# Performance work log

Measured on AMD Instinct MI355X. Metric: run time of the kernel, lower is better.

## Reference

```python
import jax, jax.numpy as jnp
import numpy as np

EPS_LOG = 1e-8
EPS_CHECK = 1e-4


def to_float8(x, exp_bits=4, mant_bits=3):
    # fp8 emulation: sign/abs/log2/floor/clamp/round chain
    max_exp = 2 ** (exp_bits - 1) - 1
    min_exp = -max_exp
    scale = 2.0 ** mant_bits
    sign = jnp.sign(x)
    x_abs = jnp.abs(x)
    exp = jnp.clip(jnp.floor(jnp.log2(x_abs + EPS_LOG)), min_exp, max_exp)
    pow2 = jnp.exp2(exp)
    mant = x_abs / pow2 - 1.0
    mant_q = jnp.round(mant * scale) / scale
    return sign * (1.0 + mant_q) * pow2


def checksum_verify(left, right, epsilon=EPS_CHECK):
    # ABFT: augment left with a column-sum row, right with a row-sum column
    left_cs = jnp.concatenate([left, jnp.sum(left, axis=0, keepdims=True)], axis=0)
    right_cs = jnp.concatenate([right, jnp.sum(right, axis=1, keepdims=True)], axis=1)
    prod_cs = left_cs @ right_cs  # [(m+1), (n+1)]
    output = prod_cs[:-1, :-1]
    row_sum_check = prod_cs[:-1, -1]
    col_sum_check = prod_cs[-1, :-1]
    col_diff = jnp.abs(jnp.sum(output, axis=0) - col_sum_check)
    row_diff = jnp.abs(jnp.sum(output, axis=1) - row_sum_check)
    mask = (row_diff > epsilon)[:, None] & (col_diff > epsilon)[None, :]
    return output, mask


def setup_inputs() -> dict:
    key = jax.random.key(0)
    kx, ku, kA, kB, kC = jax.random.split(key, 5)
    batch, n, m, p = 4096, 2048, 1024, 1024
    return {
        "x": jax.random.normal(kx, (batch, n), dtype=jnp.float32),
        "u": jax.random.normal(ku, (batch, m), dtype=jnp.float32),
        "A": jax.random.normal(kA, (n, n), dtype=jnp.float32),
        "B": jax.random.normal(kB, (n, m), dtype=jnp.float32),
        "C": jax.random.normal(kC, (p, n), dtype=jnp.float32),
    }


def reference(x, u, A, B, C):
    int_bits, frac_bits = 4, 3
    Aq = to_float8(A, int_bits, frac_bits)
    Bq = to_float8(B, int_bits, frac_bits)
    left_term, left_mask = checksum_verify(x, Aq.T)
    right_term, right_mask = checksum_verify(u, Bq.T)
    x_next = to_float8(left_term + right_term, int_bits, frac_bits)
    _ = left_mask | right_mask  # mask computed but discarded in forward (as in torch)
    Cq = to_float8(C, int_bits, frac_bits)
    y = to_float8(x_next @ Cq.T, int_bits, frac_bits)
    return (x_next, y)
```

## Files before the change

### kernel.cpp

```cpp
#include <hip/hip_runtime.h>
#include <hip/hip_bf16.h>
#include <stdint.h>

typedef __bf16 bf16_t;
typedef __attribute__((ext_vector_type(8))) __bf16 bf16x8;
typedef __attribute__((ext_vector_type(4))) __bf16 bf16x4;
typedef __attribute__((ext_vector_type(4))) float f32x4;

__device__ __forceinline__ float q8(float v) {
    float a = __builtin_fabsf(v);
    float z = a + 1e-8f;
    int ei = ((__float_as_int(z) >> 23) & 0xff) - 127;
    ei = ei > 7 ? 7 : (ei < -7 ? -7 : ei);
    float p  = __int_as_float((ei + 127) << 23);
    float ip = __int_as_float((127 - ei) << 23);
    float m  = __builtin_fmaf(a, ip, -1.0f);
    float mq = __builtin_rintf(m * 8.0f) * 0.125f;
    float r  = (1.0f + mq) * p;
    return v < 0.0f ? -r : r;
}

__device__ __forceinline__ void gload_lds16(const bf16_t* g, bf16_t* l) {
    __builtin_amdgcn_global_load_lds(
        (__attribute__((address_space(1))) void*)(g),
        (__attribute__((address_space(3))) void*)(l), 16, 0, 0);
}

__global__ void pack_all(const float* __restrict__ x, const float* __restrict__ u,
                         const float* __restrict__ A, const float* __restrict__ B,
                         const float* __restrict__ C,
                         bf16_t* __restrict__ XU, bf16_t* __restrict__ AB,
                         bf16_t* __restrict__ CQ) {
    unsigned bid = blockIdx.x;
    if (bid < 12288u) {
        unsigned row = bid / 3u, piece = bid - row * 3u;
        int col = (piece * 256 + threadIdx.x) * 4;
        float4 v;
        if (col < 2048) v = *(const float4*)&x[(size_t)row * 2048 + col];
        else            v = *(const float4*)&u[(size_t)row * 1024 + (col - 2048)];
        bf16x4 o = { (bf16_t)v.x, (bf16_t)v.y, (bf16_t)v.z, (bf16_t)v.w };
        *(bf16x4*)&XU[(size_t)row * 3072 + col] = o;
    } else if (bid < 18432u) {
        unsigned b = bid - 12288u;
        unsigned row = b / 3u, piece = b - row * 3u;
        int col = (piece * 256 + threadIdx.x) * 4;
        float4 v;
        if (col < 2048) v = *(const float4*)&A[(size_t)row * 2048 + col];
        else            v = *(const float4*)&B[(size_t)row * 1024 + (col - 2048)];
        bf16x4 o = { (bf16_t)q8(v.x), (bf16_t)q8(v.y), (bf16_t)q8(v.z), (bf16_t)q8(v.w) };
        *(bf16x4*)&AB[(size_t)row * 3072 + col] = o;
    } else {
        unsigned b = bid - 18432u;
        unsigned row = b >> 1, piece = b & 1u;
        int col = (piece * 256 + threadIdx.x) * 4;
        float4 v = *(const float4*)&C[(size_t)row * 2048 + col];
        bf16x4 o = { (bf16_t)q8(v.x), (bf16_t)q8(v.y), (bf16_t)q8(v.z), (bf16_t)q8(v.w) };
        *(bf16x4*)&CQ[(size_t)row * 2048 + col] = o;
    }
}

template<int BN, bool DUAL>
__global__ __launch_bounds__(512, 4)
void gemm_q8_kernel(const bf16_t* __restrict__ A, const bf16_t* __restrict__ B,
                    float* __restrict__ outf, bf16_t* __restrict__ outb,
                    int M, int N, int K) {
    constexpr int BM = 128;
    constexpr int BK = 128;
    constexpr int NI = BN / 32;
    constexpr int A_ITS = BM * (BK / 8) / 512;
    constexpr int B_ITS = BN * (BK / 8) / 512;

    __shared__ alignas(16) bf16_t sA[BM * BK];
    __shared__ alignas(16) bf16_t sB[BN * BK];

    const int tid  = threadIdx.x;
    const int lane = tid & 63;
    const int wave = tid >> 6;
    const int wm   = wave & 3;
    const int wn   = wave >> 2;
    const int ln16 = lane & 15;
    const int quad = lane >> 4;

    const int b   = blockIdx.x;
    const int xcd = b & 7;
    const int g   = b >> 3;
    const int bx  = (xcd & 1) * 8 + (g & 7);
    const int by  = (xcd >> 1) * 8 + (g >> 3);
    const int brow = by * BM;
    const int bcol = bx * BN;

    const bf16_t* gA[A_ITS];
#pragma unroll
    for (int it = 0; it < A_ITS; ++it) {
        int L = it * 512 + tid;
        int r = L >> 4, c = L & 15;
        gA[it] = A + (size_t)(brow + r) * K + (c ^ (r & 15)) * 8;
    }
    const bf16_t* gB[B_ITS];
#pragma unroll
    for (int it = 0; it < B_ITS; ++it) {
        int L = it * 512 + tid;
        int r = L >> 4, c = L & 15;
        gB[it] = B + (size_t)(bcol + r) * K + (c ^ (r & 15)) * 8;
    }

    int a_off[2][4], b_off[NI][4];
#pragma unroll
    for (int im = 0; im < 2; ++im) {
        int r = wm * 32 + im * 16 + ln16;
#pragma unroll
        for (int s = 0; s < 4; ++s) {
            int cg = s * 4 + quad;
            a_off[im][s] = (r * 16 + (cg ^ (r & 15))) * 8;
        }
    }
#pragma unroll
    for (int in = 0; in < NI; ++in) {
        int r = wn * (BN / 2) + in * 16 + ln16;
#pragma unroll
        for (int s = 0; s < 4; ++s) {
            int cg = s * 4 + quad;
            b_off[in][s] = (r * 16 + (cg ^ (r & 15))) * 8;
        }
    }

    f32x4 acc[2][NI];
#pragma unroll
    for (int im = 0; im < 2; ++im)
#pragma unroll
        for (int in = 0; in < NI; ++in)
            acc[im][in] = (f32x4){0.f, 0.f, 0.f, 0.f};

    for (int kt = 0; kt < K; kt += BK) {
#pragma unroll
        for (int it = 0; it < A_ITS; ++it) {
            gload_lds16(gA[it], sA + (it * 512 + wave * 64) * 8);
            gA[it] += BK;
        }
#pragma unroll
        for (int it = 0; it < B_ITS; ++it) {
            gload_lds16(gB[it], sB + (it * 512 + wave * 64) * 8);
            gB[it] += BK;
        }
        __syncthreads();
#pragma unroll
        for (int s = 0; s < 4; ++s) {
            bf16x8 af[2], bfv[NI];
#pragma unroll
            for (int im = 0; im < 2; ++im) af[im]  = *(const bf16x8*)(sA + a_off[im][s]);
#pragma unroll
            for (int in = 0; in < NI; ++in) bfv[in] = *(const bf16x8*)(sB + b_off[in][s]);
#pragma unroll
            for (int im = 0; im < 2; ++im)
#pragma unroll
                for (int in = 0; in < NI; ++in)
                    acc[im][in] = __builtin_amdgcn_mfma_f32_16x16x32_bf16(
                        af[im], bfv[in], acc[im][in], 0, 0, 0);
        }
        __syncthreads();
    }

    const int rbase = quad * 4;
#pragma unroll
    for (int im = 0; im < 2; ++im) {
#pragma unroll
        for (int in = 0; in < NI; ++in) {
            int gm = brow + wm * 32 + im * 16 + rbase;
            int gn = bcol + wn * (BN / 2) + in * 16 + ln16;
#pragma unroll
            for (int r = 0; r < 4; ++r) {
                float v = q8(acc[im][in][r]);
                outf[(size_t)(gm + r) * N + gn] = v;
                if (DUAL) outb[(size_t)(gm + r) * N + gn] = (bf16_t)v;
            }
        }
    }
}

extern "C" void kernel_launch(void* const* d_in, const int* in_sizes, int n_in,
                              void* d_out, int out_size, void* d_ws, size_t ws_size,
                              hipStream_t stream) {
    const float* x = (const float*)d_in[0];
    const float* u = (const float*)d_in[1];
    const float* A = (const float*)d_in[2];
    const float* B = (const float*)d_in[3];
    const float* C = (const float*)d_in[4];

    float* outf = (float*)d_out;
    float* xnf  = outf;
    float* yf   = outf + (size_t)4096 * 2048;

    uint8_t* ws = (uint8_t*)d_ws;
    bf16_t* XU = (bf16_t*)ws;
    bf16_t* AB = (bf16_t*)(ws + (size_t)25165824);
    bf16_t* CQ = (bf16_t*)(ws + (size_t)25165824 + 12582912);
    bf16_t* XN = (bf16_t*)(ws + (size_t)25165824 + 12582912 + 4194304);

    pack_all<<<dim3(20480), 256, 0, stream>>>(x, u, A, B, C, XU, AB, CQ);

    gemm_q8_kernel<128, true><<<dim3(512), 512, 0, stream>>>(
        XU, AB, xnf, XN, 4096, 2048, 3072);
    gemm_q8_kernel<64, false><<<dim3(512), 512, 0, stream>>>(
        XN, CQ, yf, nullptr, 4096, 1024, 2048);
}
```

Measured before the change: 200.6 us.

## Double-buffer GEMM LDS tiles with BK=64 and widen pack loads to 8 elements

The GEMM kernel now keeps two LDS stages with BK=64 and prefetches the next tile while computing the current one, using vmcnt waits and raw barriers in place of a load-then-sync loop. It also raises s_setprio during the MFMA work. The second GEMM switches to 128x128 tiles, which halves its grid to 256 blocks, and the pack kernel handles 8 elements per thread. The aim is to hide global-to-LDS latency and cut per-block overhead, at the cost of more LDS per block, a lower-occupancy second GEMM, and hand-counted waits that must stay correct.

After: 212.0 us. 5.7% more time.

```diff
diff --git a/kernel.cpp b/kernel.cpp
--- a/kernel.cpp
+++ b/kernel.cpp
@@ -4,7 +4,6 @@
 
 typedef __bf16 bf16_t;
 typedef __attribute__((ext_vector_type(8))) __bf16 bf16x8;
-typedef __attribute__((ext_vector_type(4))) __bf16 bf16x4;
 typedef __attribute__((ext_vector_type(4))) float f32x4;
 
 __device__ __forceinline__ float q8(float v) {
@@ -26,52 +25,66 @@
         (__attribute__((address_space(3))) void*)(l), 16, 0, 0);
 }
 
+__device__ __forceinline__ bf16x8 cvt8(float4 a, float4 b) {
+    bf16x8 o = { (bf16_t)a.x, (bf16_t)a.y, (bf16_t)a.z, (bf16_t)a.w,
+                 (bf16_t)b.x, (bf16_t)b.y, (bf16_t)b.z, (bf16_t)b.w };
+    return o;
+}
+__device__ __forceinline__ bf16x8 q8x8(float4 a, float4 b) {
+    bf16x8 o = { (bf16_t)q8(a.x), (bf16_t)q8(a.y), (bf16_t)q8(a.z), (bf16_t)q8(a.w),
+                 (bf16_t)q8(b.x), (bf16_t)q8(b.y), (bf16_t)q8(b.z), (bf16_t)q8(b.w) };
+    return o;
+}
+
 __global__ void pack_all(const float* __restrict__ x, const float* __restrict__ u,
                          const float* __restrict__ A, const float* __restrict__ B,
                          const float* __restrict__ C,
                          bf16_t* __restrict__ XU, bf16_t* __restrict__ AB,
                          bf16_t* __restrict__ CQ) {
-    unsigned bid = blockIdx.x;
-    if (bid < 12288u) {
-        unsigned row = bid / 3u, piece = bid - row * 3u;
-        int col = (piece * 256 + threadIdx.x) * 4;
-        float4 v;
-        if (col < 2048) v = *(const float4*)&x[(size_t)row * 2048 + col];
-        else            v = *(const float4*)&u[(size_t)row * 1024 + (col - 2048)];
-        bf16x4 o = { (bf16_t)v.x, (bf16_t)v.y, (bf16_t)v.z, (bf16_t)v.w };
-        *(bf16x4*)&XU[(size_t)row * 3072 + col] = o;
-    } else if (bid < 18432u) {
-        unsigned b = bid - 12288u;
-        unsigned row = b / 3u, piece = b - row * 3u;
-        int col = (piece * 256 + threadIdx.x) * 4;
-        float4 v;
-        if (col < 2048) v = *(const float4*)&A[(size_t)row * 2048 + col];
-        else            v = *(const float4*)&B[(size_t)row * 1024 + (col - 2048)];
-        bf16x4 o = { (bf16_t)q8(v.x), (bf16_t)q8(v.y), (bf16_t)q8(v.z), (bf16_t)q8(v.w) };
-        *(bf16x4*)&AB[(size_t)row * 3072 + col] = o;
+    const unsigned bid = blockIdx.x;
+    const int tid = threadIdx.x;
+    if (bid < 4096u) {
+        size_t r = bid; int col = tid * 8;
+        float4 v0 = *(const float4*)&x[r * 2048 + col];
+        float4 v1 = *(const float4*)&x[r * 2048 + col + 4];
+        *(bf16x8*)&XU[r * 3072 + col] = cvt8(v0, v1);
+    } else if (bid < 6144u) {
+        unsigned b = bid - 4096u;
+        size_t r = b * 2 + (tid >> 7); int col = (tid & 127) * 8;
+        float4 v0 = *(const float4*)&u[r * 1024 + col];
+        float4 v1 = *(const float4*)&u[r * 1024 + col + 4];
+        *(bf16x8*)&XU[r * 3072 + 2048 + col] = cvt8(v0, v1);
+    } else if (bid < 8192u) {
+        size_t r = bid - 6144u; int col = tid * 8;
+        float4 v0 = *(const float4*)&A[r * 2048 + col];
+        float4 v1 = *(const float4*)&A[r * 2048 + col + 4];
+        *(bf16x8*)&AB[r * 3072 + col] = q8x8(v0, v1);
+    } else if (bid < 9216u) {
+        unsigned b = bid - 8192u;
+        size_t r = b * 2 + (tid >> 7); int col = (tid & 127) * 8;
+        float4 v0 = *(const float4*)&B[r * 1024 + col];
+        float4 v1 = *(const float4*)&B[r * 1024 + col + 4];
+        *(bf16x8*)&AB[r * 3072 + 2048 + col] = q8x8(v0, v1);
     } else {
-        unsigned b = bid - 18432u;
-        unsigned row = b >> 1, piece = b & 1u;
-        int col = (piece * 256 + threadIdx.x) * 4;
-        float4 v = *(const float4*)&C[(size_t)row * 2048 + col];
-        bf16x4 o = { (bf16_t)q8(v.x), (bf16_t)q8(v.y), (bf16_t)q8(v.z), (bf16_t)q8(v.w) };
-        *(bf16x4*)&CQ[(size_t)row * 2048 + col] = o;
-    }
-}
-
-template<int BN, bool DUAL>
+        size_t r = bid - 9216u; int col = tid * 8;
+        float4 v0 = *(const float4*)&C[r * 2048 + col];
+        float4 v1 = *(const float4*)&C[r * 2048 + col + 4];
+        *(bf16x8*)&CQ[r * 2048 + col] = q8x8(v0, v1);
+    }
+}
+
+template<int NBX, bool DUAL>
 __global__ __launch_bounds__(512, 4)
 void gemm_q8_kernel(const bf16_t* __restrict__ A, const bf16_t* __restrict__ B,
                     float* __restrict__ outf, bf16_t* __restrict__ outb,
                     int M, int N, int K) {
     constexpr int BM = 128;
-    constexpr int BK = 128;
-    constexpr int NI = BN / 32;
-    constexpr int A_ITS = BM * (BK / 8) / 512;
-    constexpr int B_ITS = BN * (BK / 8) / 512;
-
-    __shared__ alignas(16) bf16_t sA[BM * BK];
-    __shared__ alignas(16) bf16_t sB[BN * BK];
+    constexpr int BN = 128;
+    constexpr int BK = 64;
+    constexpr int PX = NBX / 2;
+
+    __shared__ alignas(16) bf16_t sA[2][BM * BK];
+    __shared__ alignas(16) bf16_t sB[2][BN * BK];
 
     const int tid  = threadIdx.x;
     const int lane = tid & 63;
@@ -84,89 +97,108 @@
     const int b   = blockIdx.x;
     const int xcd = b & 7;
     const int g   = b >> 3;
-    const int bx  = (xcd & 1) * 8 + (g & 7);
-    const int by  = (xcd >> 1) * 8 + (g >> 3);
+    const int bx  = (xcd & 1) * PX + (g % PX);
+    const int by  = (xcd >> 1) * 8 + (g / PX);
     const int brow = by * BM;
     const int bcol = bx * BN;
 
-    const bf16_t* gA[A_ITS];
-#pragma unroll
-    for (int it = 0; it < A_ITS; ++it) {
+    const bf16_t* gA[2];
+    const bf16_t* gB[2];
+#pragma unroll
+    for (int it = 0; it < 2; ++it) {
         int L = it * 512 + tid;
-        int r = L >> 4, c = L & 15;
-        gA[it] = A + (size_t)(brow + r) * K + (c ^ (r & 15)) * 8;
-    }
-    const bf16_t* gB[B_ITS];
-#pragma unroll
-    for (int it = 0; it < B_ITS; ++it) {
-        int L = it * 512 + tid;
-        int r = L >> 4, c = L & 15;
-        gB[it] = B + (size_t)(bcol + r) * K + (c ^ (r & 15)) * 8;
-    }
-
-    int a_off[2][4], b_off[NI][4];
+        int r = L >> 3, c = L & 7;
+        gA[it] = A + (size_t)(brow + r) * K + (c ^ (r & 7)) * 8;
+        gB[it] = B + (size_t)(bcol + r) * K + (c ^ (r & 7)) * 8;
+    }
+
+    int a_off[2][2], b_off[4][2];
 #pragma unroll
     for (int im = 0; im < 2; ++im) {
         int r = wm * 32 + im * 16 + ln16;
 #pragma unroll
-        for (int s = 0; s < 4; ++s) {
+        for (int s = 0; s < 2; ++s) {
             int cg = s * 4 + quad;
-            a_off[im][s] = (r * 16 + (cg ^ (r & 15))) * 8;
-        }
-    }
-#pragma unroll
-    for (int in = 0; in < NI; ++in) {
-        int r = wn * (BN / 2) + in * 16 + ln16;
-#pragma unroll
-        for (int s = 0; s < 4; ++s) {
+            a_off[im][s] = (r * 8 + (cg ^ (r & 7))) * 8;
+        }
+    }
+#pragma unroll
+    for (int in = 0; in < 4; ++in) {
+        int r = wn * 64 + in * 16 + ln16;
+#pragma unroll
+        for (int s = 0; s < 2; ++s) {
             int cg = s * 4 + quad;
-            b_off[in][s] = (r * 16 + (cg ^ (r & 15))) * 8;
-        }
-    }
-
-    f32x4 acc[2][NI];
+            b_off[in][s] = (r * 8 + (cg ^ (r & 7))) * 8;
+        }
+    }
+
+    f32x4 acc[2][4];
 #pragma unroll
     for (int im = 0; im < 2; ++im)
 #pragma unroll
-        for (int in = 0; in < NI; ++in)
+        for (int in = 0; in < 4; ++in)
             acc[im][in] = (f32x4){0.f, 0.f, 0.f, 0.f};
 
-    for (int kt = 0; kt < K; kt += BK) {
-#pragma unroll
-        for (int it = 0; it < A_ITS; ++it) {
-            gload_lds16(gA[it], sA + (it * 512 + wave * 64) * 8);
+    auto stage_tile = [&](int cur) {
+#pragma unroll
+        for (int it = 0; it < 2; ++it) {
+            gload_lds16(gA[it], &sA[cur][(it * 512 + wave * 64) * 8]);
             gA[it] += BK;
         }
 #pragma unroll
-        for (int it = 0; it < B_ITS; ++it) {
-            gload_lds16(gB[it], sB + (it * 512 + wave * 64) * 8);
+        for (int it = 0; it < 2; ++it) {
+            gload_lds16(gB[it], &sB[cur][(it * 512 + wave * 64) * 8]);
             gB[it] += BK;
         }
-        __syncthreads();
-#pragma unroll
-        for (int s = 0; s < 4; ++s) {
-            bf16x8 af[2], bfv[NI];
-#pragma unroll
-            for (int im = 0; im < 2; ++im) af[im]  = *(const bf16x8*)(sA + a_off[im][s]);
-#pragma unroll
-            for (int in = 0; in < NI; ++in) bfv[in] = *(const bf16x8*)(sB + b_off[in][s]);
+    };
+
+    auto compute_tile = [&](int cur) {
+        const bf16_t* bA = sA[cur];
+        const bf16_t* bB = sB[cur];
+        __builtin_amdgcn_s_setprio(1);
+#pragma unroll
+        for (int s = 0; s < 2; ++s) {
+            bf16x8 af[2], bfv[4];
+#pragma unroll
+            for (int im = 0; im < 2; ++im) af[im]  = *(const bf16x8*)(bA + a_off[im][s]);
+#pragma unroll
+            for (int in = 0; in < 4; ++in) bfv[in] = *(const bf16x8*)(bB + b_off[in][s]);
 #pragma unroll
             for (int im = 0; im < 2; ++im)
 #pragma unroll
-                for (int in = 0; in < NI; ++in)
+                for (int in = 0; in < 4; ++in)
                     acc[im][in] = __builtin_amdgcn_mfma_f32_16x16x32_bf16(
                         af[im], bfv[in], acc[im][in], 0, 0, 0);
         }
-        __syncthreads();
-    }
+        __builtin_amdgcn_s_setprio(0);
+    };
+
+    stage_tile(0);
+    stage_tile(1);
+
+    const int NT = K / BK;
+    for (int t = 0; t < NT - 1; ++t) {
+        const int cur = t & 1;
+        asm volatile("s_waitcnt vmcnt(4)" ::: "memory");
+        __builtin_amdgcn_s_barrier();
+        asm volatile("" ::: "memory");
+        compute_tile(cur);
+        asm volatile("" ::: "memory");
+        __builtin_amdgcn_s_barrier();
+        if (t + 2 < NT) stage_tile(cur);
+    }
+    asm volatile("s_waitcnt vmcnt(0)" ::: "memory");
+    __builtin_amdgcn_s_barrier();
+    asm volatile("" ::: "memory");
+    compute_tile((NT - 1) & 1);
 
     const int rbase = quad * 4;
 #pragma unroll
     for (int im = 0; im < 2; ++im) {
 #pragma unroll
-        for (int in = 0; in < NI; ++in) {
+        for (int in = 0; in < 4; ++in) {
             int gm = brow + wm * 32 + im * 16 + rbase;
-            int gn = bcol + wn * (BN / 2) + in * 16 + ln16;
+            int gn = bcol + wn * 64 + in * 16 + ln16;
 #pragma unroll
             for (int r = 0; r < 4; ++r) {
                 float v = q8(acc[im][in][r]);
@@ -196,10 +228,10 @@
     bf16_t* CQ = (bf16_t*)(ws + (size_t)25165824 + 12582912);
     bf16_t* XN = (bf16_t*)(ws + (size_t)25165824 + 12582912 + 4194304);
 
-    pack_all<<<dim3(20480), 256, 0, stream>>>(x, u, A, B, C, XU, AB, CQ);
-
-    gemm_q8_kernel<128, true><<<dim3(512), 512, 0, stream>>>(
+    pack_all<<<dim3(10240), 256, 0, stream>>>(x, u, A, B, C, XU, AB, CQ);
+
+    gemm_q8_kernel<16, true><<<dim3(512), 512, 0, stream>>>(
         XU, AB, xnf, XN, 4096, 2048, 3072);
-    gemm_q8_kernel<64, false><<<dim3(512), 512, 0, stream>>>(
+    gemm_q8_kernel<8, false><<<dim3(256), 512, 0, stream>>>(
         XN, CQ, yf, nullptr, 4096, 1024, 2048);
 }
```
